# Optimization experiments

Hardware: AMD Instinct MI355X
Metric: run time of the kernel (lower is better)

Reference implementation:

```python
import jax, jax.numpy as jnp
import numpy as np

B = 64
D_MODEL = 2048
D_SSM = 4096      # expand * d_model
HEADDIM = 64
NHEADS = 64       # D_SSM // HEADDIM
D_STATE = 128
D_IN_PROJ = 2 * D_SSM + 2 * D_STATE + NHEADS  # 8512, d_mlp == 0
ACT_LEVELS = 2 ** (8 - 1) - 1  # 127
W_LEVELS = 2 ** (8 - 1) - 1


def fake_quant(x, levels):
    # symmetric absmax fake-quant along last dim with straight-through estimator
    scale = jnp.max(jnp.abs(x), axis=-1, keepdims=True) / levels
    scale = jnp.where(scale == 0, 1.0, scale)
    q = jnp.round(x / scale) * scale
    return x + jax.lax.stop_gradient(q - x)


def quant_linear(x, W):
    # QuantLinear: fake-quant activations (per row) and weights (per output channel)
    xq = fake_quant(x, ACT_LEVELS)
    Wq = fake_quant(W, W_LEVELS)
    return xq @ Wq.T


def softplus_taylor3(x):
    return jnp.log(2.0) + 0.5 * x + x ** 2 / 8.0 + x ** 3 / 48.0


def exp_taylor5(x):
    return 1.0 + x + x ** 2 / 2.0 + x ** 3 / 6.0 + x ** 4 / 24.0 + x ** 5 / 120.0


def setup_inputs() -> dict:
    key = jax.random.key(0)
    k = jax.random.split(key, 7)
    hidden_states = jax.random.normal(k[0], (B, 1, D_MODEL), dtype=jnp.float32)
    ssm_state = jax.random.normal(k[1], (B, NHEADS, HEADDIM, D_STATE), dtype=jnp.float32) * 0.1
    W_in = jax.random.normal(k[2], (D_IN_PROJ, D_MODEL), dtype=jnp.float32) * (1.0 / np.sqrt(D_MODEL))
    # dt_bias = inverse-softplus of dt ~ LogUniform(1e-3, 1e-1)
    dt = jnp.exp(jax.random.uniform(k[3], (NHEADS,)) * (np.log(0.1) - np.log(0.001)) + np.log(0.001))
    dt_bias = dt + jnp.log(-jnp.expm1(-dt))
    A_log = jnp.log(jax.random.uniform(k[4], (NHEADS,), minval=1.0, maxval=16.0))
    Dp = jnp.ones((D_SSM,), dtype=jnp.float32)
    W_out = jax.random.normal(k[5], (D_MODEL, D_SSM), dtype=jnp.float32) * (1.0 / np.sqrt(D_SSM))
    return {"hidden_states": hidden_states, "ssm_state": ssm_state, "W_in": W_in,
            "dt_bias": dt_bias, "A_log": A_log, "D": Dp, "W_out": W_out}


def reference(hidden_states, ssm_state, W_in, dt_bias, A_log, D, W_out):
    dtype = hidden_states.dtype
    b = hidden_states.shape[0]
    zxbcdt = quant_linear(hidden_states[:, 0, :], W_in)  # [b, 8512]
    z = zxbcdt[:, :D_SSM]
    xBC = zxbcdt[:, D_SSM:2 * D_SSM + 2 * D_STATE]
    dt = zxbcdt[:, -NHEADS:]
    # activation fake-quant on xBC (STE)
    xBC = fake_quant(xBC, ACT_LEVELS)
    x = xBC[:, :D_SSM]                                   # [b, d_ssm]
    Bm = xBC[:, D_SSM:D_SSM + D_STATE]                   # [b, n]
    C = xBC[:, D_SSM + D_STATE:]                         # [b, n]
    A = -jnp.exp(A_log.astype(jnp.float32))              # [h]
    # no_sftplus: piecewise 3rd-order Taylor softplus
    dt = dt + dt_bias.astype(dt.dtype)
    dt = jnp.where(dt < -2.0, 0.0, jnp.where(dt > 2.0, dt, softplus_taylor3(dt)))
    # taylor_exp: clipped 5th-order Taylor exp of dt*A
    dA = jnp.maximum(dt * A, -10000.0)
    scale = jnp.clip(exp_taylor5(dA), 0.0, 1.0)          # [b, h]
    xh = x.reshape(b, NHEADS, HEADDIM)                   # [b, h, p]
    dBx = jnp.einsum('bh,bn,bhp->bhpn', dt, Bm, xh)
    ssm_state = ssm_state * scale[:, :, None, None] + dBx  # [b, h, p, n]
    y = jnp.einsum('bhpn,bn->bhp', ssm_state.astype(dtype), C).reshape(b, D_SSM)
    y = fake_quant(y, ACT_LEVELS)
    y = y + D.astype(dtype) * x                          # per-channel skip (D has d_ssm entries)
    y = y * jax.nn.relu(z)
    y = fake_quant(y, ACT_LEVELS)
    out = quant_linear(y, W_out)                         # [b, d_model]
    return out[:, None, :]
```

## Files before the change

### kernel.cpp

```cpp
#include <hip/hip_runtime.h>


#define B_       64
#define DMODEL   2048
#define DSSM     4096
#define NH       64
#define HD       64
#define DSTATE   128
#define DPROJ    8512
#define XBCLEN   4352
#define KS1      2
#define KS2      4

typedef __attribute__((ext_vector_type(4))) int int4v;

__device__ __forceinline__ float blockMax256(float v, float* sm) {
  #pragma unroll
  for (int off = 32; off > 0; off >>= 1)
    v = fmaxf(v, __shfl_xor(v, off, 64));
  __syncthreads();
  if ((threadIdx.x & 63) == 0) sm[threadIdx.x >> 6] = v;
  __syncthreads();
  return fmaxf(fmaxf(sm[0], sm[1]), fmaxf(sm[2], sm[3]));
}

__device__ __forceinline__ float absmax4(float4 v) {
  return fmaxf(fmaxf(fabsf(v.x), fabsf(v.y)), fmaxf(fabsf(v.z), fabsf(v.w)));
}

__device__ __forceinline__ unsigned int pack4(float a, float b, float c, float d,
                                              float rs) {
  int c0 = (int)rintf(a * rs), c1 = (int)rintf(b * rs);
  int c2 = (int)rintf(c * rs), c3 = (int)rintf(d * rs);
  return (unsigned)(c0 & 255) | ((unsigned)(c1 & 255) << 8) |
         ((unsigned)(c2 & 255) << 16) | ((unsigned)(c3 & 255) << 24);
}

template<int COLS>
__device__ __forceinline__ void qrow8(const float* __restrict__ in,
                                      unsigned int* __restrict__ outq,
                                      float* __restrict__ scales, int r, float* sm) {
  constexpr int NV = COLS / 1024;
  const float4* row = (const float4*)(in + (size_t)r * COLS);
  float4 v[NV];
  float m = 0.f;
  #pragma unroll
  for (int i = 0; i < NV; i++) {
    v[i] = row[threadIdx.x + i * 256];
    m = fmaxf(m, absmax4(v[i]));
  }
  float mx = blockMax256(m, sm);
  float s = mx * (1.0f / 127.0f);
  float rs = (s == 0.f) ? 0.f : 127.0f / mx;
  if (s == 0.f) s = 1.f;
  if (threadIdx.x == 0) scales[r] = s;
  unsigned int* orow = outq + (size_t)r * (COLS / 4);
  #pragma unroll
  for (int i = 0; i < NV; i++)
    orow[threadIdx.x + i * 256] = pack4(v[i].x, v[i].y, v[i].z, v[i].w, rs);
}

__global__ __launch_bounds__(256) void kquant_all(
    const float* __restrict__ hidden, const float* __restrict__ W_in,
    const float* __restrict__ W_out,
    unsigned int* __restrict__ xq, unsigned int* __restrict__ winq,
    unsigned int* __restrict__ woq,
    float* __restrict__ sx, float* __restrict__ swin, float* __restrict__ swo) {
  __shared__ float sm[4];
  int bid = blockIdx.x;
  if (bid < DPROJ)                 qrow8<DMODEL>(W_in, winq, swin, bid, sm);
  else if (bid < DPROJ + DMODEL)   qrow8<DSSM>(W_out, woq, swo, bid - DPROJ, sm);
  else                             qrow8<DMODEL>(hidden, xq, sx, bid - DPROJ - DMODEL, sm);
}

__global__ __launch_bounds__(256) void gemm_q8(
    const char* __restrict__ A, int lda, const float* __restrict__ sA,
    const char* __restrict__ Bq, int ldb, const float* __restrict__ sB,
    float* __restrict__ Pout, int N, int kchunk) {
  int wave = threadIdx.x >> 6;
  int lane = threadIdx.x & 63;
  int l16 = lane & 15, quad = lane >> 4;
  int n0 = blockIdx.x * 64 + wave * 16;
  int k0 = blockIdx.y * kchunk;
  int4v zero = {0, 0, 0, 0};
  int4v acc[4] = {zero, zero, zero, zero};
  const char* brow = Bq + (size_t)(n0 + l16) * ldb + quad * 16;
  const char* arow = A + (size_t)l16 * lda + quad * 16;
  int4v bnext = *(const int4v*)(brow + k0);
  int4v anext[4];
  #pragma unroll
  for (int mt = 0; mt < 4; mt++)
    anext[mt] = *(const int4v*)(arow + (size_t)mt * 16 * lda + k0);
  for (int k = k0; k < k0 + kchunk; k += 64) {
    int4v bcur = bnext;
    int4v acur[4] = {anext[0], anext[1], anext[2], anext[3]};
    if (k + 64 < k0 + kchunk) {
      bnext = *(const int4v*)(brow + k + 64);
      #pragma unroll
      for (int mt = 0; mt < 4; mt++)
        anext[mt] = *(const int4v*)(arow + (size_t)mt * 16 * lda + k + 64);
    }
    #pragma unroll
    for (int mt = 0; mt < 4; mt++)
      acc[mt] = __builtin_amdgcn_mfma_i32_16x16x64_i8(acur[mt], bcur, acc[mt], 0, 0, 0);
  }
  int ncol = n0 + l16;
  float sb = sB[ncol];
  float* pbase = Pout + (size_t)blockIdx.y * 64 * N;
  #pragma unroll
  for (int mt = 0; mt < 4; mt++) {
    #pragma unroll
    for (int r = 0; r < 4; r++) {
      int m = mt * 16 + quad * 4 + r;
      pbase[(size_t)m * N + ncol] = (float)acc[mt][r] * sA[m] * sb;
    }
  }
}

__global__ __launch_bounds__(256) void kmid(
    const float* __restrict__ P1, const float* __restrict__ dt_bias,
    const float* __restrict__ A_log,
    float* __restrict__ zbuf, float* __restrict__ xbcq, float* __restrict__ coefs) {
  __shared__ float sm[4];
  __shared__ float dts[NH];
  __shared__ float sbc;
  int b = blockIdx.x, t = threadIdx.x;
  float4 v[9];
  float m = 0.f;
  #pragma unroll
  for (int i = 0; i < 9; i++) {
    int idx = t + i * 256;
    if (idx < 2128) {
      const float4* p0 = (const float4*)P1 + (size_t)b * 2128 + idx;
      float4 a = p0[0];
      #pragma unroll
      for (int s = 1; s < KS1; s++) {
        float4 q = p0[(size_t)s * 64 * 2128];
        a.x += q.x; a.y += q.y; a.z += q.z; a.w += q.w;
      }
      v[i] = a;
      if (idx >= 1024 && idx < 2112) m = fmaxf(m, absmax4(a));
      if (idx >= 2112) {
        dts[(t - 64) * 4 + 0] = a.x;
        dts[(t - 64) * 4 + 1] = a.y;
        dts[(t - 64) * 4 + 2] = a.z;
        dts[(t - 64) * 4 + 3] = a.w;
      }
    }
  }
  float mx = blockMax256(m, sm);
  float s = mx * (1.0f / 127.0f);
  float rs = (s == 0.f) ? 0.f : 127.0f / mx;
  if (s == 0.f) s = 1.f;
  float4 q8 = {0.f, 0.f, 0.f, 0.f};
  #pragma unroll
  for (int i = 0; i < 9; i++) {
    int idx = t + i * 256;
    if (idx < 1024) {
      *((float4*)(zbuf + (size_t)b * DSSM) + idx) = v[i];
    } else if (idx < 2112) {
      float4 q;
      q.x = rintf(v[i].x * rs) * s;
      q.y = rintf(v[i].y * rs) * s;
      q.z = rintf(v[i].z * rs) * s;
      q.w = rintf(v[i].w * rs) * s;
      if (i == 8) q8 = q;
      *((float4*)(xbcq + (size_t)b * XBCLEN) + (idx - 1024)) = q;
    }
  }
  float4 oth;
  oth.x = __shfl(q8.x, (t & 63) ^ 32, 64);
  oth.y = __shfl(q8.y, (t & 63) ^ 32, 64);
  oth.z = __shfl(q8.z, (t & 63) ^ 32, 64);
  oth.w = __shfl(q8.w, (t & 63) ^ 32, 64);
  float p = 0.f;
  if (t < 32) p = q8.x * oth.x + q8.y * oth.y + q8.z * oth.z + q8.w * oth.w;
  #pragma unroll
  for (int off = 1; off < 32; off <<= 1) p += __shfl_xor(p, off, 64);
  if (t == 0) sbc = p;
  __syncthreads();
  if (t < NH) {
    float dtv = dts[t] + dt_bias[t];
    if (dtv < -2.f) dtv = 0.f;
    else if (dtv <= 2.f)
      dtv = 0.6931471805599453f + 0.5f * dtv + dtv * dtv * (1.f / 8.f)
            + dtv * dtv * dtv * (1.f / 48.f);
    float A = -expf(A_log[t]);
    float dA = fmaxf(dtv * A, -10000.f);
    float e = 1.f + dA + dA * dA * (1.f / 2.f) + dA * dA * dA * (1.f / 6.f)
              + dA * dA * dA * dA * (1.f / 24.f)
              + dA * dA * dA * dA * dA * (1.f / 120.f);
    e = fminf(fmaxf(e, 0.f), 1.f);
    coefs[((size_t)b * NH + t) * 2 + 0] = e;
    coefs[((size_t)b * NH + t) * 2 + 1] = dtv * sbc;
  }
}

__global__ __launch_bounds__(256) void ky(const float* __restrict__ state,
                                          const float* __restrict__ xbcq,
                                          const float* __restrict__ coefs,
                                          float* __restrict__ yraw) {
  int h = blockIdx.x, b = blockIdx.y, t = threadIdx.x;
  const float* xrow = xbcq + (size_t)b * XBCLEN;
  const float* Cv = xrow + DSSM + DSTATE;
  float4 c4 = *(const float4*)(Cv + (t & 31) * 4);
  float2 cf = *(const float2*)(coefs + ((size_t)b * NH + h) * 2);
  const float4* st = (const float4*)(state + ((size_t)b * NH + h) * (HD * DSTATE));
  #pragma unroll
  for (int j = 0; j < 8; j++) {
    float4 s4 = st[j * 256 + t];
    float acc = s4.x * c4.x + s4.y * c4.y + s4.z * c4.z + s4.w * c4.w;
    #pragma unroll
    for (int off = 1; off < 32; off <<= 1) acc += __shfl_xor(acc, off, 64);
    if ((t & 31) == 0) {
      int r = j * 8 + (t >> 5);
      int d = h * HD + r;
      yraw[(size_t)b * DSSM + d] = cf.x * acc + cf.y * xrow[d];
    }
  }
}

__global__ __launch_bounds__(256) void kepi(const float* __restrict__ yraw,
                                            const float* __restrict__ zbuf,
                                            const float* __restrict__ xbcq,
                                            const float* __restrict__ Dv,
                                            unsigned int* __restrict__ q3,
                                            float* __restrict__ sy) {
  __shared__ float sm[4];
  int b = blockIdx.x, t = threadIdx.x;
  const float* yrow = yraw + (size_t)b * DSSM;
  float4 yv[4];
  float m = 0.f;
  #pragma unroll
  for (int i = 0; i < 4; i++) {
    yv[i] = *(const float4*)(yrow + t * 4 + i * 1024);
    m = fmaxf(m, absmax4(yv[i]));
  }
  float mx1 = blockMax256(m, sm);
  float s1 = mx1 * (1.0f / 127.0f);
  float rs1 = (s1 == 0.f) ? 0.f : 127.0f / mx1;
  if (s1 == 0.f) s1 = 1.f;
  float4 y3[4];
  float m2 = 0.f;
  #pragma unroll
  for (int i = 0; i < 4; i++) {
    int idx = t * 4 + i * 1024;
    float4 x4 = *(const float4*)(xbcq + (size_t)b * XBCLEN + idx);
    float4 z4 = *(const float4*)(zbuf + (size_t)b * DSSM + idx);
    float4 d4 = *(const float4*)(Dv + idx);
    float4 r;
    r.x = (rintf(yv[i].x * rs1) * s1 + d4.x * x4.x) * fmaxf(z4.x, 0.f);
    r.y = (rintf(yv[i].y * rs1) * s1 + d4.y * x4.y) * fmaxf(z4.y, 0.f);
    r.z = (rintf(yv[i].z * rs1) * s1 + d4.z * x4.z) * fmaxf(z4.z, 0.f);
    r.w = (rintf(yv[i].w * rs1) * s1 + d4.w * x4.w) * fmaxf(z4.w, 0.f);
    y3[i] = r;
    m2 = fmaxf(m2, absmax4(r));
  }
  float mx3 = blockMax256(m2, sm);
  float s3 = mx3 * (1.0f / 127.0f);
  float rs3 = (s3 == 0.f) ? 0.f : 127.0f / mx3;
  if (s3 == 0.f) s3 = 1.f;
  if (t == 0) sy[b] = s3;
  unsigned int* orow = q3 + (size_t)b * (DSSM / 4);
  #pragma unroll
  for (int i = 0; i < 4; i++)
    orow[t + i * 256] = pack4(y3[i].x, y3[i].y, y3[i].z, y3[i].w, rs3);
}

__global__ __launch_bounds__(256) void kout(const float* __restrict__ P2,
                                            float* __restrict__ out) {
  int idx = blockIdx.x * 256 + threadIdx.x;
  const float4* p = (const float4*)P2;
  float4 s = p[idx];
  #pragma unroll
  for (int i = 1; i < KS2; i++) {
    float4 a = p[(size_t)i * 32768 + idx];
    s.x += a.x; s.y += a.y; s.z += a.z; s.w += a.w;
  }
  ((float4*)out)[idx] = s;
}

extern "C" void kernel_launch(void* const* d_in, const int* in_sizes, int n_in,
                              void* d_out, int out_size, void* d_ws, size_t ws_size,
                              hipStream_t stream) {
  const float* hidden  = (const float*)d_in[0];
  const float* ssm     = (const float*)d_in[1];
  const float* W_in    = (const float*)d_in[2];
  const float* dt_bias = (const float*)d_in[3];
  const float* A_log   = (const float*)d_in[4];
  const float* Dv      = (const float*)d_in[5];
  const float* W_out   = (const float*)d_in[6];
  float* out = (float*)d_out;

  char* p = (char*)d_ws;
  auto alloc = [&](size_t bytes) {
    char* r = p;
    p += (bytes + 255) & ~(size_t)255;
    return r;
  };
  unsigned int* xq   = (unsigned int*)alloc((size_t)B_ * DMODEL);
  unsigned int* winq = (unsigned int*)alloc((size_t)DPROJ * DMODEL);
  unsigned int* woq  = (unsigned int*)alloc((size_t)DMODEL * DSSM);
  unsigned int* q3   = (unsigned int*)alloc((size_t)B_ * DSSM);
  float* sx    = (float*)alloc(B_ * 4);
  float* swin  = (float*)alloc(DPROJ * 4);
  float* swo   = (float*)alloc(DMODEL * 4);
  float* sy    = (float*)alloc(B_ * 4);
  float* P1    = (float*)alloc((size_t)KS1 * B_ * DPROJ * 4);
  float* P2    = (float*)alloc((size_t)KS2 * B_ * DMODEL * 4);
  float* zbuf  = (float*)alloc((size_t)B_ * DSSM * 4);
  float* xbcq  = (float*)alloc((size_t)B_ * XBCLEN * 4);
  float* coefs = (float*)alloc((size_t)B_ * NH * 2 * 4);
  float* yraw  = (float*)alloc((size_t)B_ * DSSM * 4);

  kquant_all<<<DPROJ + DMODEL + B_, 256, 0, stream>>>(hidden, W_in, W_out,
                                                      xq, winq, woq, sx, swin, swo);
  gemm_q8<<<dim3(DPROJ / 64, KS1), 256, 0, stream>>>((const char*)xq, DMODEL, sx,
                                                     (const char*)winq, DMODEL, swin,
                                                     P1, DPROJ, DMODEL / KS1);
  kmid<<<B_, 256, 0, stream>>>(P1, dt_bias, A_log, zbuf, xbcq, coefs);
  ky<<<dim3(NH, B_), 256, 0, stream>>>(ssm, xbcq, coefs, yraw);
  kepi<<<B_, 256, 0, stream>>>(yraw, zbuf, xbcq, Dv, q3, sy);
  gemm_q8<<<dim3(DMODEL / 64, KS2), 256, 0, stream>>>((const char*)q3, DSSM, sy,
                                                      (const char*)woq, DSSM, swo,
                                                      P2, DMODEL, DSSM / KS2);
  kout<<<DMODEL / 16, 256, 0, stream>>>(P2, out);
}
```

Measured before the change: 311.5 us.

## Fuse weight fake-quant into int8 GEMMs and drop split-K reduction

Weights are now read as fp32 inside each GEMM block, quantized per output row into shared memory, and consumed directly by int8 MFMA. This removes the separate weight-quantization kernel, the global int8 weight round trip, the split-K partial buffers and the final reduction kernel. In exchange, the out-projection uses only 4 of 16 MFMA columns per block, and each block serializes its quantization before compute.

```diff
diff --git a/kernel.cpp b/kernel.cpp
--- a/kernel.cpp
+++ b/kernel.cpp
@@ -9,8 +9,7 @@
 #define DSTATE   128
 #define DPROJ    8512
 #define XBCLEN   4352
-#define KS1      2
-#define KS2      4
+#define KS1      1
 
 typedef __attribute__((ext_vector_type(4))) int int4v;
 
@@ -36,16 +35,16 @@
          ((unsigned)(c2 & 255) << 16) | ((unsigned)(c3 & 255) << 24);
 }
 
-template<int COLS>
-__device__ __forceinline__ void qrow8(const float* __restrict__ in,
-                                      unsigned int* __restrict__ outq,
-                                      float* __restrict__ scales, int r, float* sm) {
-  constexpr int NV = COLS / 1024;
-  const float4* row = (const float4*)(in + (size_t)r * COLS);
-  float4 v[NV];
+__global__ __launch_bounds__(256) void quantx(const float* __restrict__ in,
+                                              unsigned int* __restrict__ outq,
+                                              float* __restrict__ scales) {
+  __shared__ float sm[4];
+  int r = blockIdx.x;
+  const float4* row = (const float4*)(in + (size_t)r * DMODEL);
+  float4 v[2];
   float m = 0.f;
   #pragma unroll
-  for (int i = 0; i < NV; i++) {
+  for (int i = 0; i < 2; i++) {
     v[i] = row[threadIdx.x + i * 256];
     m = fmaxf(m, absmax4(v[i]));
   }
@@ -54,65 +53,72 @@
   float rs = (s == 0.f) ? 0.f : 127.0f / mx;
   if (s == 0.f) s = 1.f;
   if (threadIdx.x == 0) scales[r] = s;
-  unsigned int* orow = outq + (size_t)r * (COLS / 4);
-  #pragma unroll
-  for (int i = 0; i < NV; i++)
+  unsigned int* orow = outq + (size_t)r * (DMODEL / 4);
+  #pragma unroll
+  for (int i = 0; i < 2; i++)
     orow[threadIdx.x + i * 256] = pack4(v[i].x, v[i].y, v[i].z, v[i].w, rs);
 }
 
-__global__ __launch_bounds__(256) void kquant_all(
-    const float* __restrict__ hidden, const float* __restrict__ W_in,
-    const float* __restrict__ W_out,
-    unsigned int* __restrict__ xq, unsigned int* __restrict__ winq,
-    unsigned int* __restrict__ woq,
-    float* __restrict__ sx, float* __restrict__ swin, float* __restrict__ swo) {
-  __shared__ float sm[4];
-  int bid = blockIdx.x;
-  if (bid < DPROJ)                 qrow8<DMODEL>(W_in, winq, swin, bid, sm);
-  else if (bid < DPROJ + DMODEL)   qrow8<DSSM>(W_out, woq, swo, bid - DPROJ, sm);
-  else                             qrow8<DMODEL>(hidden, xq, sx, bid - DPROJ - DMODEL, sm);
-}
-
-__global__ __launch_bounds__(256) void gemm_q8(
-    const char* __restrict__ A, int lda, const float* __restrict__ sA,
-    const char* __restrict__ Bq, int ldb, const float* __restrict__ sB,
-    float* __restrict__ Pout, int N, int kchunk) {
-  int wave = threadIdx.x >> 6;
-  int lane = threadIdx.x & 63;
+template<int K, int ROWS>
+__global__ __launch_bounds__(256) void fgemm(const float* __restrict__ W,
+                                             const char* __restrict__ Aq,
+                                             const float* __restrict__ sA,
+                                             float* __restrict__ Cout, int N) {
+  constexpr int NF4 = K / 256;
+  constexpr int RPW = ROWS / 4;
+  constexpr int LSTRIDE = K / 4 + 4;
+  __shared__ unsigned int wq[ROWS * LSTRIDE];
+  __shared__ float smax[ROWS];
+  int t = threadIdx.x, wave = t >> 6, lane = t & 63;
+  int n0 = blockIdx.x * ROWS;
+  #pragma unroll
+  for (int rr = 0; rr < RPW; rr++) {
+    int row = wave * RPW + rr;
+    const float4* rp = (const float4*)(W + (size_t)(n0 + row) * K);
+    float4 v[NF4];
+    float m = 0.f;
+    #pragma unroll
+    for (int c = 0; c < NF4; c++) {
+      v[c] = rp[lane + c * 64];
+      m = fmaxf(m, absmax4(v[c]));
+    }
+    #pragma unroll
+    for (int off = 32; off > 0; off >>= 1)
+      m = fmaxf(m, __shfl_xor(m, off, 64));
+    float s = (m == 0.f) ? 1.f : m * (1.0f / 127.0f);
+    float rs = (m == 0.f) ? 0.f : 127.0f / m;
+    if (lane == 0) smax[row] = s;
+    unsigned int* wrow = wq + row * LSTRIDE;
+    #pragma unroll
+    for (int c = 0; c < NF4; c++)
+      wrow[lane + c * 64] = pack4(v[c].x, v[c].y, v[c].z, v[c].w, rs);
+  }
+  __syncthreads();
   int l16 = lane & 15, quad = lane >> 4;
-  int n0 = blockIdx.x * 64 + wave * 16;
-  int k0 = blockIdx.y * kchunk;
-  int4v zero = {0, 0, 0, 0};
-  int4v acc[4] = {zero, zero, zero, zero};
-  const char* brow = Bq + (size_t)(n0 + l16) * ldb + quad * 16;
-  const char* arow = A + (size_t)l16 * lda + quad * 16;
-  int4v bnext = *(const int4v*)(brow + k0);
-  int4v anext[4];
-  #pragma unroll
-  for (int mt = 0; mt < 4; mt++)
-    anext[mt] = *(const int4v*)(arow + (size_t)mt * 16 * lda + k0);
-  for (int k = k0; k < k0 + kchunk; k += 64) {
-    int4v bcur = bnext;
-    int4v acur[4] = {anext[0], anext[1], anext[2], anext[3]};
-    if (k + 64 < k0 + kchunk) {
-      bnext = *(const int4v*)(brow + k + 64);
-      #pragma unroll
-      for (int mt = 0; mt < 4; mt++)
-        anext[mt] = *(const int4v*)(arow + (size_t)mt * 16 * lda + k + 64);
-    }
-    #pragma unroll
-    for (int mt = 0; mt < 4; mt++)
-      acc[mt] = __builtin_amdgcn_mfma_i32_16x16x64_i8(acur[mt], bcur, acc[mt], 0, 0, 0);
-  }
-  int ncol = n0 + l16;
-  float sb = sB[ncol];
-  float* pbase = Pout + (size_t)blockIdx.y * 64 * N;
-  #pragma unroll
-  for (int mt = 0; mt < 4; mt++) {
+  int4v acc = {0, 0, 0, 0};
+  const char* arow = Aq + (size_t)(wave * 16 + l16) * K + quad * 16;
+  const unsigned int* brow = wq + l16 * LSTRIDE + quad * 4;
+  for (int k = 0; k < K; k += 256) {
+    int4v af[4], bf[4];
+    #pragma unroll
+    for (int u = 0; u < 4; u++)
+      af[u] = *(const int4v*)(arow + k + u * 64);
+    #pragma unroll
+    for (int u = 0; u < 4; u++) {
+      int4v z = {0, 0, 0, 0};
+      bf[u] = z;
+      if (l16 < ROWS) bf[u] = *(const int4v*)(brow + (k + u * 64) / 4);
+    }
+    #pragma unroll
+    for (int u = 0; u < 4; u++)
+      acc = __builtin_amdgcn_mfma_i32_16x16x64_i8(af[u], bf[u], acc, 0, 0, 0);
+  }
+  if (l16 < ROWS) {
+    float sw = smax[l16];
     #pragma unroll
     for (int r = 0; r < 4; r++) {
-      int m = mt * 16 + quad * 4 + r;
-      pbase[(size_t)m * N + ncol] = (float)acc[mt][r] * sA[m] * sb;
+      int m = wave * 16 + quad * 4 + r;
+      Cout[(size_t)m * N + n0 + l16] = (float)acc[r] * sA[m] * sw;
     }
   }
 }
@@ -267,19 +273,6 @@
     orow[t + i * 256] = pack4(y3[i].x, y3[i].y, y3[i].z, y3[i].w, rs3);
 }
 
-__global__ __launch_bounds__(256) void kout(const float* __restrict__ P2,
-                                            float* __restrict__ out) {
-  int idx = blockIdx.x * 256 + threadIdx.x;
-  const float4* p = (const float4*)P2;
-  float4 s = p[idx];
-  #pragma unroll
-  for (int i = 1; i < KS2; i++) {
-    float4 a = p[(size_t)i * 32768 + idx];
-    s.x += a.x; s.y += a.y; s.z += a.z; s.w += a.w;
-  }
-  ((float4*)out)[idx] = s;
-}
-
 extern "C" void kernel_launch(void* const* d_in, const int* in_sizes, int n_in,
                               void* d_out, int out_size, void* d_ws, size_t ws_size,
                               hipStream_t stream) {
@@ -298,31 +291,22 @@
     p += (bytes + 255) & ~(size_t)255;
     return r;
   };
-  unsigned int* xq   = (unsigned int*)alloc((size_t)B_ * DMODEL);
-  unsigned int* winq = (unsigned int*)alloc((size_t)DPROJ * DMODEL);
-  unsigned int* woq  = (unsigned int*)alloc((size_t)DMODEL * DSSM);
-  unsigned int* q3   = (unsigned int*)alloc((size_t)B_ * DSSM);
+  unsigned int* xq = (unsigned int*)alloc((size_t)B_ * DMODEL);
+  unsigned int* q3 = (unsigned int*)alloc((size_t)B_ * DSSM);
   float* sx    = (float*)alloc(B_ * 4);
-  float* swin  = (float*)alloc(DPROJ * 4);
-  float* swo   = (float*)alloc(DMODEL * 4);
   float* sy    = (float*)alloc(B_ * 4);
-  float* P1    = (float*)alloc((size_t)KS1 * B_ * DPROJ * 4);
-  float* P2    = (float*)alloc((size_t)KS2 * B_ * DMODEL * 4);
+  float* zxb   = (float*)alloc((size_t)B_ * DPROJ * 4);
   float* zbuf  = (float*)alloc((size_t)B_ * DSSM * 4);
   float* xbcq  = (float*)alloc((size_t)B_ * XBCLEN * 4);
   float* coefs = (float*)alloc((size_t)B_ * NH * 2 * 4);
   float* yraw  = (float*)alloc((size_t)B_ * DSSM * 4);
 
-  kquant_all<<<DPROJ + DMODEL + B_, 256, 0, stream>>>(hidden, W_in, W_out,
-                                                      xq, winq, woq, sx, swin, swo);
-  gemm_q8<<<dim3(DPROJ / 64, KS1), 256, 0, stream>>>((const char*)xq, DMODEL, sx,
-                                                     (const char*)winq, DMODEL, swin,
-                                                     P1, DPROJ, DMODEL / KS1);
-  kmid<<<B_, 256, 0, stream>>>(P1, dt_bias, A_log, zbuf, xbcq, coefs);
+  quantx<<<B_, 256, 0, stream>>>(hidden, xq, sx);
+  fgemm<DMODEL, 16><<<DPROJ / 16, 256, 0, stream>>>(W_in, (const char*)xq, sx,
+                                                    zxb, DPROJ);
+  kmid<<<B_, 256, 0, stream>>>(zxb, dt_bias, A_log, zbuf, xbcq, coefs);
   ky<<<dim3(NH, B_), 256, 0, stream>>>(ssm, xbcq, coefs, yraw);
   kepi<<<B_, 256, 0, stream>>>(yraw, zbuf, xbcq, Dv, q3, sy);
-  gemm_q8<<<dim3(DMODEL / 64, KS2), 256, 0, stream>>>((const char*)q3, DSSM, sy,
-                                                      (const char*)woq, DSSM, swo,
-                                                      P2, DMODEL, DSSM / KS2);
-  kout<<<DMODEL / 16, 256, 0, stream>>>(P2, out);
-}
+  fgemm<DSSM, 4><<<DMODEL / 4, 256, 0, stream>>>(W_out, (const char*)q3, sy,
+                                                 out, DMODEL);
+}
```

New measurement: 307.8 us. Within noise of the previous version (-1.2%).
